# Performance work log

Hardware: AMD Instinct MI355X
Metric: run time of the kernel (lower is better)

Reference implementation:

```python
import jax, jax.numpy as jnp
import numpy as np
import math

N_HEAD = 16
D_MODEL = 1024
ATT_DIM = D_MODEL // N_HEAD


def setup_inputs() -> dict:
    key = jax.random.key(0)
    ks = jax.random.split(key, 11)
    B, T, D = 2, 2048, D_MODEL
    s = 1.0 / math.sqrt(D)
    return {
        "q": jax.random.normal(ks[0], (B, T, D), jnp.float32),
        "k": jax.random.normal(ks[1], (B, T, D), jnp.float32),
        "v": jax.random.normal(ks[2], (B, T, D), jnp.float32),
        "Wq": jax.random.normal(ks[3], (D, D), jnp.float32) * s,
        "bq": jnp.zeros((D,), jnp.float32),
        "Wk": jax.random.normal(ks[4], (D, D), jnp.float32) * s,
        "bk": jnp.zeros((D,), jnp.float32),
        "Wv": jax.random.normal(ks[5], (D, D), jnp.float32) * s,
        "bv": jnp.zeros((D,), jnp.float32),
        "Wo": jax.random.normal(ks[6], (D, D), jnp.float32) * s,
        "bo": jnp.zeros((D,), jnp.float32),
    }


def reference(q, k, v, Wq, bq, Wk, bk, Wv, bv, Wo, bo):
    B, T, D = q.shape
    H, hd = N_HEAD, ATT_DIM
    # Linear projections (torch Linear: x @ W.T + b)
    qh = (q @ Wq.T + bq).reshape(B, T, H, hd).transpose(0, 2, 1, 3)  # [B,H,T,hd]
    kh = (k @ Wk.T + bk).reshape(B, T, H, hd).transpose(0, 2, 1, 3)
    vh = (v @ Wv.T + bv).reshape(B, T, H, hd).transpose(0, 2, 1, 3)
    scale = 1.0 / math.sqrt(hd)
    score = jnp.einsum("bhqd,bhkd->bhqk", qh, kh) * scale  # [B,H,T,T]
    attn = jax.nn.softmax(score, axis=-1)
    out = jnp.einsum("bhqk,bhkd->bhqd", attn, vh)  # [B,H,T,hd]
    out = out.transpose(0, 2, 1, 3).reshape(B, T, D)
    return out @ Wo.T + bo
```

## Files before the change

kernel.cpp:

```cpp
#include <hip/hip_runtime.h>


typedef __attribute__((ext_vector_type(8))) short bf16x8;
typedef __attribute__((ext_vector_type(4))) float f32x4;
typedef __attribute__((ext_vector_type(4))) unsigned int u32x4;

#define E22 ((size_t)1 << 22)
#define E20 ((size_t)1 << 20)

__device__ __forceinline__ unsigned short f2bf(float x) {
    unsigned int u = __float_as_uint(x);
    u += 0x7fffu + ((u >> 16) & 1u);
    return (unsigned short)(u >> 16);
}
__device__ __forceinline__ unsigned int pk2bf(float a, float b) {
    return __builtin_amdgcn_perm(__float_as_uint(a), __float_as_uint(b), 0x03020706u);
}
__device__ __forceinline__ void gl16(const void* g, void* l) {
    __builtin_amdgcn_global_load_lds(
        (const __attribute__((address_space(1))) void*)g,
        (__attribute__((address_space(3))) void*)l, 16, 0, 0);
}
__device__ __forceinline__ f32x4 mfma16(bf16x8 a, bf16x8 b, f32x4 c) {
    return __builtin_amdgcn_mfma_f32_16x16x32_bf16(a, b, c, 0, 0, 0);
}

__global__ __launch_bounds__(256)
void split_all(const float* __restrict__ q, const float* __restrict__ k,
               const float* __restrict__ v, const float* __restrict__ wq,
               const float* __restrict__ wk, const float* __restrict__ wv,
               const float* __restrict__ wo, unsigned short* __restrict__ ws)
{
    const size_t t = (size_t)blockIdx.x * 256 + threadIdx.x;
    const size_t e = t * 4;
    const float* src; unsigned short* dst; size_t off;
    if (e < 3 * E22) {
        const unsigned int which = (unsigned int)(e >> 22);
        src = which == 0 ? q : (which == 1 ? k : v);
        off = e & (E22 - 1);
        dst = ws + (size_t)which * E22;
    } else {
        const size_t e2 = e - 3 * E22;
        const unsigned int which = (unsigned int)(e2 >> 20);
        off = e2 & (E20 - 1);
        src = which == 0 ? wq : (which == 1 ? wk : (which == 2 ? wv : wo));
        dst = ws + 3 * E22 + (size_t)which * E20;
    }
    const float4 xv = *(const float4*)(src + off);
    ushort4 h4;
    h4.x = f2bf(xv.x); h4.y = f2bf(xv.y); h4.z = f2bf(xv.z); h4.w = f2bf(xv.w);
    *(ushort4*)(dst + off) = h4;
}

__global__ __launch_bounds__(512)
void gemm_qkv(const unsigned short* __restrict__ Xall,
              const unsigned short* __restrict__ Wcat,
              const float* __restrict__ bq, const float* __restrict__ bk,
              const float* __restrict__ bv, unsigned short* __restrict__ Qhp,
              unsigned short* __restrict__ Khp, unsigned short* __restrict__ Vtp)
{
    __shared__ unsigned short Xs[3 * 4096], Ws[3 * 4096];
    const int tid = threadIdx.x;
    const int w = tid >> 6, ln = tid & 63;
    const int quad = ln >> 4, L = ln & 15;
    const int wy = w >> 1, wx = w & 1;

    const int bid = blockIdx.x;
    const int xcd = bid & 7, j = bid >> 3;
    const int gg = xcd * 12 + (j >> 3);
    const int which = gg >> 5, m_i = gg & 31, n_i = j & 7;
    const int m0 = m_i * 128;

    const unsigned short* X = Xall + (size_t)which * E22;
    const unsigned short* W = Wcat + ((size_t)which * 1024 + n_i * 128) * 1024;
    const float* bp = which == 0 ? bq : (which == 1 ? bk : bv);
    unsigned short* outp = which == 0 ? Qhp : (which == 1 ? Khp : Vtp);
    const float qscale = which == 0 ? 0.18033688011f : 1.0f;

    const int ci  = w * 64 + ln;
    const int row = ci >> 2;
    const int gc  = (ci & 3) ^ ((row >> 1) & 3);
    const int lb  = w * 1024;
    const unsigned short* Xbp = X + (size_t)m0 * 1024;
    const size_t gx = (size_t)row * 1024 + gc * 8;

    f32x4 acc[2][4];
#pragma unroll
    for (int i = 0; i < 2; ++i)
#pragma unroll
        for (int jj = 0; jj < 4; ++jj) { f32x4 z = {0.f,0.f,0.f,0.f}; acc[i][jj] = z; }

#define QSTAGE(k0_, bo_)                                                       \
    do {                                                                       \
        gl16(Xbp + gx + (k0_), (char*)Xs + (bo_) + lb);                        \
        gl16(W   + gx + (k0_), (char*)Ws + (bo_) + lb);                        \
    } while (0)

#define QCOMP(eo_)                                                             \
    do {                                                                       \
        const unsigned short* Xc = Xs + (eo_);                                 \
        const unsigned short* Wc = Ws + (eo_);                                 \
        bf16x8 ah[2], bh[4];                                                   \
        _Pragma("unroll")                                                      \
        for (int mt = 0; mt < 2; ++mt) {                                       \
            const int rr = wy * 32 + mt * 16 + L;                              \
            ah[mt] = *(const bf16x8*)(Xc + rr * 32 +                           \
                                      ((quad ^ ((rr >> 1) & 3)) * 8));         \
        }                                                                      \
        _Pragma("unroll")                                                      \
        for (int nt = 0; nt < 4; ++nt) {                                       \
            const int rr = wx * 64 + nt * 16 + L;                              \
            bh[nt] = *(const bf16x8*)(Wc + rr * 32 +                           \
                                      ((quad ^ ((rr >> 1) & 3)) * 8));         \
        }                                                                      \
        _Pragma("unroll")                                                      \
        for (int mt = 0; mt < 2; ++mt)                                         \
            _Pragma("unroll")                                                  \
            for (int nt = 0; nt < 4; ++nt)                                     \
                acc[mt][nt] = mfma16(ah[mt], bh[nt], acc[mt][nt]);             \
    } while (0)

    QSTAGE(0, 0);
    QSTAGE(32, 8192);

    int cur = 0;
    for (int kt = 0; kt < 31; ++kt) {
        asm volatile("s_waitcnt vmcnt(2)" ::: "memory");
        __builtin_amdgcn_s_barrier();
        asm volatile("" ::: "memory");
        if (kt < 30) {
            int st = cur + 2; if (st >= 3) st -= 3;
            QSTAGE((kt + 2) * 32, st * 8192);
        }
        QCOMP(cur * 4096);
        cur = (cur == 2) ? 0 : cur + 1;
    }
    asm volatile("s_waitcnt vmcnt(0)" ::: "memory");
    __builtin_amdgcn_s_barrier();
    asm volatile("" ::: "memory");
    QCOMP(cur * 4096);
#undef QSTAGE
#undef QCOMP

#pragma unroll
    for (int mt = 0; mt < 2; ++mt)
#pragma unroll
        for (int nt = 0; nt < 4; ++nt) {
            const int gm0 = m0 + wy * 32 + mt * 16 + quad * 4;
            const int bn  = n_i * 128 + wx * 64 + nt * 16 + L;
            const float bvv = bp[bn];
            const int hh = bn >> 6, dd = bn & 63;
            if (which < 2) {
#pragma unroll
                for (int r = 0; r < 4; ++r) {
                    const int gm = gm0 + r;
                    const int bb = gm >> 11, tt = gm & 2047;
                    outp[((size_t)(bb * 16 + hh) * 2048 + tt) * 64 + dd] =
                        f2bf((acc[mt][nt][r] + bvv) * qscale);
                }
            } else {
                const int bb = gm0 >> 11, t0 = gm0 & 2047;
                const int c5 = t0 & 31;
                const int p0 = (t0 & ~31) | (((c5 & 15) >> 2) << 3) | ((c5 >> 4) << 2);
                ushort4 pk;
                pk.x = f2bf(acc[mt][nt][0] + bvv);
                pk.y = f2bf(acc[mt][nt][1] + bvv);
                pk.z = f2bf(acc[mt][nt][2] + bvv);
                pk.w = f2bf(acc[mt][nt][3] + bvv);
                *(ushort4*)(outp + ((size_t)(bb * 16 + hh) * 64 + dd) * 2048 + p0) = pk;
            }
        }
}

__global__ __launch_bounds__(256)
void gemm_out(const unsigned short* __restrict__ X, const unsigned short* __restrict__ W,
              const float* __restrict__ bias, float* __restrict__ outp)
{
    __shared__ unsigned short Xs[3 * 4096], Ws[3 * 2048];
    const int tid = threadIdx.x;
    const int w = tid >> 6, ln = tid & 63;
    const int quad = ln >> 4, L = ln & 15;

    const int bid = blockIdx.x;
    const int xcd = bid & 7, j = bid >> 3;
    const int m0 = (xcd * 4 + (j >> 4)) * 128;
    const int n0 = (j & 15) * 64;

    const int cix0 = ln, cix1 = 64 + ln;
    const int rowx0 = w * 32 + (cix0 >> 2), rowx1 = w * 32 + (cix1 >> 2);
    const int gcx0 = (cix0 & 3) ^ ((rowx0 >> 1) & 3);
    const int gcx1 = (cix1 & 3) ^ ((rowx1 >> 1) & 3);
    const int roww = w * 16 + (ln >> 2);
    const int gcw = (ln & 3) ^ ((roww >> 1) & 3);
    const size_t gxx0 = (size_t)(m0 + rowx0) * 1024 + gcx0 * 8;
    const size_t gxx1 = (size_t)(m0 + rowx1) * 1024 + gcx1 * 8;
    const size_t gww  = (size_t)(n0 + roww) * 1024 + gcw * 8;

    f32x4 acc[2][4];
#pragma unroll
    for (int i = 0; i < 2; ++i)
#pragma unroll
        for (int jj = 0; jj < 4; ++jj) { f32x4 z = {0.f,0.f,0.f,0.f}; acc[i][jj] = z; }

#define OSTAGE(k0_, bf_)                                                       \
    do {                                                                       \
        gl16(X + gxx0 + (k0_), (char*)Xs + (bf_) * 8192 + w * 2048);           \
        gl16(X + gxx1 + (k0_), (char*)Xs + (bf_) * 8192 + w * 2048 + 1024);    \
        gl16(W + gww  + (k0_), (char*)Ws + (bf_) * 4096 + w * 1024);           \
    } while (0)

#define OCOMP(bf_)                                                             \
    do {                                                                       \
        const unsigned short* Xc = Xs + (bf_) * 4096;                          \
        const unsigned short* Wc = Ws + (bf_) * 2048;                          \
        bf16x8 ah[2], bh[4];                                                   \
        _Pragma("unroll")                                                      \
        for (int mt = 0; mt < 2; ++mt) {                                       \
            const int row = w * 32 + mt * 16 + L;                              \
            ah[mt] = *(const bf16x8*)(Xc + row * 32 +                          \
                                      ((quad ^ ((row >> 1) & 3)) * 8));        \
        }                                                                      \
        _Pragma("unroll")                                                      \
        for (int nt = 0; nt < 4; ++nt) {                                       \
            const int row = nt * 16 + L;                                       \
            bh[nt] = *(const bf16x8*)(Wc + row * 32 +                          \
                                      ((quad ^ ((row >> 1) & 3)) * 8));        \
        }                                                                      \
        _Pragma("unroll")                                                      \
        for (int mt = 0; mt < 2; ++mt)                                         \
            _Pragma("unroll")                                                  \
            for (int nt = 0; nt < 4; ++nt)                                     \
                acc[mt][nt] = mfma16(ah[mt], bh[nt], acc[mt][nt]);             \
    } while (0)

    OSTAGE(0, 0);
    OSTAGE(32, 1);

    int cur = 0;
    for (int kt = 0; kt < 31; ++kt) {
        asm volatile("s_waitcnt vmcnt(3)" ::: "memory");
        __builtin_amdgcn_s_barrier();
        asm volatile("" ::: "memory");
        if (kt < 30) {
            int st = cur + 2; if (st >= 3) st -= 3;
            OSTAGE((kt + 2) * 32, st);
        }
        OCOMP(cur);
        cur = (cur == 2) ? 0 : cur + 1;
    }
    asm volatile("s_waitcnt vmcnt(0)" ::: "memory");
    __builtin_amdgcn_s_barrier();
    asm volatile("" ::: "memory");
    OCOMP(cur);
#undef OSTAGE
#undef OCOMP

#pragma unroll
    for (int mt = 0; mt < 2; ++mt)
#pragma unroll
        for (int nt = 0; nt < 4; ++nt) {
            const int gm0 = m0 + w * 32 + mt * 16 + quad * 4;
            const int gn  = n0 + nt * 16 + L;
            const float bvv = bias[gn];
#pragma unroll
            for (int r = 0; r < 4; ++r)
                outp[(size_t)(gm0 + r) * 1024 + gn] = acc[mt][nt][r] + bvv;
        }
}

__global__ __launch_bounds__(256, 2)
void flash(const unsigned short* __restrict__ Qh, const unsigned short* __restrict__ Kh,
           const unsigned short* __restrict__ Vt, unsigned short* __restrict__ A)
{
    __shared__ unsigned short SM[32768];
    __shared__ float Lsc[2 * 4 * 64];
    const int tid = threadIdx.x;
    const int w = tid >> 6, ln = tid & 63;
    const int quad = ln >> 4, L = ln & 15;
    const int wq = w & 1, wk = w >> 1;

    const int bid = blockIdx.x;
    const int xcd = bid & 7, j = bid >> 3;
    const int bh_i = xcd * 4 + (j & 3);
    const int qt = j >> 2;
    const int b = bh_i >> 4, h = bh_i & 15;

    const unsigned short* Qb = Qh + ((size_t)bh_i * 2048 + qt * 128 + wq * 64) * 64;
    const unsigned short* Kb = Kh + (size_t)bh_i * 2048 * 64;
    const unsigned short* Vb = Vt + (size_t)bh_i * 64 * 2048;

    bf16x8 bq[4][2];
#pragma unroll
    for (int nt = 0; nt < 4; ++nt)
#pragma unroll
        for (int kc = 0; kc < 2; ++kc)
            bq[nt][kc] = *(const bf16x8*)(Qb + (nt * 16 + L) * 64 + kc * 32 + quad * 8);

    const short one_bf = (short)0x3F80;
    bf16x8 bone = {one_bf, one_bf, one_bf, one_bf, one_bf, one_bf, one_bf, one_bf};

    f32x4 o[4][4];
    f32x4 lacc[4];
#pragma unroll
    for (int mtd = 0; mtd < 4; ++mtd)
#pragma unroll
        for (int nt = 0; nt < 4; ++nt) { f32x4 z = {0.f,0.f,0.f,0.f}; o[mtd][nt] = z; }
#pragma unroll
    for (int nt = 0; nt < 4; ++nt) { f32x4 z = {0.f,0.f,0.f,0.f}; lacc[nt] = z; }

    const int ci0 = (w * 2 + 0) * 64 + ln, ci1 = (w * 2 + 1) * 64 + ln;
    const int rr0 = ci0 >> 3, rr1 = ci1 >> 3;
    const int gc0 = (ci0 & 7) ^ (rr0 & 7), gc1 = (ci1 & 7) ^ (rr1 & 7);

#define STAGE1(kt_, b_, s_)                                                     \
    do {                                                                        \
        gl16(Kb + (size_t)((kt_) * 64 + rr0) * 64 + gc0 * 8,                    \
             (char*)SM + (b_) * 16384 + (s_) * 8192 + (w * 2 + 0) * 1024);      \
        gl16(Kb + (size_t)((kt_) * 64 + rr1) * 64 + gc1 * 8,                    \
             (char*)SM + (b_) * 16384 + (s_) * 8192 + (w * 2 + 1) * 1024);      \
        gl16(Vb + (size_t)rr0 * 2048 + (kt_) * 64 + gc0 * 8,                    \
             (char*)SM + 32768 + (b_) * 16384 + (s_) * 8192 + (w * 2 + 0) * 1024); \
        gl16(Vb + (size_t)rr1 * 2048 + (kt_) * 64 + gc1 * 8,                    \
             (char*)SM + 32768 + (b_) * 16384 + (s_) * 8192 + (w * 2 + 1) * 1024); \
    } while (0)

#define SUBCOMP(b_, s_)                                                         \
    do {                                                                        \
        const unsigned short* Ksb = SM + (b_) * 8192 + (s_) * 4096;             \
        const unsigned short* Vsb = SM + 16384 + (b_) * 8192 + (s_) * 4096;     \
        bf16x8 ak[2][2];                                                        \
        _Pragma("unroll")                                                       \
        for (int mt = 0; mt < 2; ++mt)                                          \
            _Pragma("unroll")                                                   \
            for (int kc = 0; kc < 2; ++kc) {                                    \
                const int row = wk * 32 + mt * 16 + L;                          \
                ak[mt][kc] = *(const bf16x8*)(Ksb + row * 64 +                  \
                                              (((kc * 4 + quad) ^ (L & 7)) * 8)); \
            }                                                                   \
        f32x4 s[2][4];                                                          \
        _Pragma("unroll")                                                       \
        for (int mt = 0; mt < 2; ++mt)                                          \
            _Pragma("unroll")                                                   \
            for (int nt = 0; nt < 4; ++nt) {                                    \
                f32x4 z = {0.f, 0.f, 0.f, 0.f};                                 \
                z = mfma16(ak[mt][0], bq[nt][0], z);                            \
                z = mfma16(ak[mt][1], bq[nt][1], z);                            \
                s[mt][nt] = z;                                                  \
            }                                                                   \
        bf16x8 pbx[4];                                                          \
        _Pragma("unroll")                                                       \
        for (int nt = 0; nt < 4; ++nt) {                                        \
            u32x4 pd;                                                           \
            pd.x = pk2bf(__builtin_amdgcn_exp2f(s[0][nt][0]),                   \
                         __builtin_amdgcn_exp2f(s[0][nt][1]));                  \
            pd.y = pk2bf(__builtin_amdgcn_exp2f(s[0][nt][2]),                   \
                         __builtin_amdgcn_exp2f(s[0][nt][3]));                  \
            pd.z = pk2bf(__builtin_amdgcn_exp2f(s[1][nt][0]),                   \
                         __builtin_amdgcn_exp2f(s[1][nt][1]));                  \
            pd.w = pk2bf(__builtin_amdgcn_exp2f(s[1][nt][2]),                   \
                         __builtin_amdgcn_exp2f(s[1][nt][3]));                  \
            pbx[nt] = __builtin_bit_cast(bf16x8, pd);                           \
        }                                                                       \
        bf16x8 av[4];                                                           \
        _Pragma("unroll")                                                       \
        for (int mtd = 0; mtd < 4; ++mtd) {                                     \
            const int row = mtd * 16 + L;                                       \
            av[mtd] = *(const bf16x8*)(Vsb + row * 64 +                         \
                                       (((wk * 4 + quad) ^ (L & 7)) * 8));      \
        }                                                                       \
        _Pragma("unroll")                                                       \
        for (int mtd = 0; mtd < 4; ++mtd)                                       \
            _Pragma("unroll")                                                   \
            for (int nt = 0; nt < 4; ++nt)                                      \
                o[mtd][nt] = mfma16(av[mtd], pbx[nt], o[mtd][nt]);              \
        _Pragma("unroll")                                                       \
        for (int nt = 0; nt < 4; ++nt)                                          \
            lacc[nt] = mfma16(bone, pbx[nt], lacc[nt]);                         \
    } while (0)

    STAGE1(0, 0, 0);
    STAGE1(1, 0, 1);

    for (int p = 0; p < 16; ++p) {
        const int cur = p & 1;
        __syncthreads();
        if (p < 15) {
            STAGE1(2 * p + 2, cur ^ 1, 0);
            STAGE1(2 * p + 3, cur ^ 1, 1);
        }
        SUBCOMP(cur, 0);
        SUBCOMP(cur, 1);
    }
#undef STAGE1
#undef SUBCOMP

    __syncthreads();
    float* Rb = (float*)SM;
    if (wk == 1) {
#pragma unroll
        for (int mtd = 0; mtd < 4; ++mtd)
#pragma unroll
            for (int nt = 0; nt < 4; ++nt)
                *(f32x4*)(Rb + wq * 4096 + (mtd * 4 + nt) * 256 + ln * 4) = o[mtd][nt];
#pragma unroll
        for (int nt = 0; nt < 4; ++nt)
            Lsc[wq * 256 + nt * 64 + ln] = lacc[nt][0];
    }
    __syncthreads();
    if (wk == 0) {
#pragma unroll
        for (int mtd = 0; mtd < 4; ++mtd)
#pragma unroll
            for (int nt = 0; nt < 4; ++nt)
                o[mtd][nt] += *(const f32x4*)(Rb + wq * 4096 + (mtd * 4 + nt) * 256 + ln * 4);

#pragma unroll
        for (int nt = 0; nt < 4; ++nt) {
            const float lsum = lacc[nt][0] + Lsc[wq * 256 + nt * 64 + ln];
            const float inv = 1.0f / lsum;
            const int qrow = b * 2048 + qt * 128 + wq * 64 + nt * 16 + L;
#pragma unroll
            for (int mtd = 0; mtd < 4; ++mtd) {
                const int d0 = mtd * 16 + quad * 4;
                ushort4 pk;
                pk.x = f2bf(o[mtd][nt][0] * inv);
                pk.y = f2bf(o[mtd][nt][1] * inv);
                pk.z = f2bf(o[mtd][nt][2] * inv);
                pk.w = f2bf(o[mtd][nt][3] * inv);
                *(ushort4*)(A + (size_t)qrow * 1024 + h * 64 + d0) = pk;
            }
        }
    }
}

extern "C" void kernel_launch(void* const* d_in, const int* in_sizes, int n_in,
                              void* d_out, int out_size, void* d_ws, size_t ws_size,
                              hipStream_t stream) {
    const float* q  = (const float*)d_in[0];
    const float* k  = (const float*)d_in[1];
    const float* v  = (const float*)d_in[2];
    const float* Wq = (const float*)d_in[3];
    const float* bq = (const float*)d_in[4];
    const float* Wk = (const float*)d_in[5];
    const float* bk = (const float*)d_in[6];
    const float* Wv = (const float*)d_in[7];
    const float* bv = (const float*)d_in[8];
    const float* Wo = (const float*)d_in[9];
    const float* bo = (const float*)d_in[10];

    unsigned short* W = (unsigned short*)d_ws;
    unsigned short *Xall = W;
    unsigned short *Wcat = W + 3 * E22;
    unsigned short *Wob  = Wcat + 3 * E20;
    unsigned short *Qhp  = W + 4 * E22;
    unsigned short *Khp  = W + 5 * E22;
    unsigned short *Vtp  = W + 6 * E22;
    unsigned short *A    = W;

    split_all<<<16384, 256, 0, stream>>>(q, k, v, Wq, Wk, Wv, Wo, W);

    gemm_qkv<<<768, 512, 0, stream>>>(Xall, Wcat, bq, bk, bv, Qhp, Khp, Vtp);

    flash<<<512, 256, 0, stream>>>(Qhp, Khp, Vtp, A);

    gemm_out<<<512, 256, 0, stream>>>(A, Wob, bo, (float*)d_out);
}
```

Baseline: 218.0 us.

## Shrink QKV GEMM tile to 128x64 with 256 threads and double buffering

The QKV projection GEMM moves from 512-thread blocks with 128x128 tiles and a three-stage async pipeline to 256-thread blocks with 128x64 tiles and two-stage double buffering, doubling the grid to 1536 blocks. The XCD-aware block mapping and load indexing are reworked to match. The intent is more blocks per CU and better load balance, at the cost of less reuse of each X tile, more global traffic, and a shallower pipeline that waits on every load with a full __syncthreads.

```diff
diff --git a/kernel.cpp b/kernel.cpp
--- a/kernel.cpp
+++ b/kernel.cpp
@@ -52,37 +52,42 @@
     *(ushort4*)(dst + off) = h4;
 }
 
-__global__ __launch_bounds__(512)
+__global__ __launch_bounds__(256)
 void gemm_qkv(const unsigned short* __restrict__ Xall,
               const unsigned short* __restrict__ Wcat,
               const float* __restrict__ bq, const float* __restrict__ bk,
               const float* __restrict__ bv, unsigned short* __restrict__ Qhp,
               unsigned short* __restrict__ Khp, unsigned short* __restrict__ Vtp)
 {
-    __shared__ unsigned short Xs[3 * 4096], Ws[3 * 4096];
+    __shared__ unsigned short Xs[2 * 4096], Ws[2 * 2048];
     const int tid = threadIdx.x;
     const int w = tid >> 6, ln = tid & 63;
     const int quad = ln >> 4, L = ln & 15;
-    const int wy = w >> 1, wx = w & 1;
 
     const int bid = blockIdx.x;
-    const int xcd = bid & 7, j = bid >> 3;
-    const int gg = xcd * 12 + (j >> 3);
-    const int which = gg >> 5, m_i = gg & 31, n_i = j & 7;
+    const int xcd = bid & 7;
+    const int g = xcd * 192 + (bid >> 3);
+    const int which = g >> 9;
+    const int rem = g & 511;
+    const int m_i = rem >> 4, n_i = rem & 15;
     const int m0 = m_i * 128;
 
     const unsigned short* X = Xall + (size_t)which * E22;
-    const unsigned short* W = Wcat + ((size_t)which * 1024 + n_i * 128) * 1024;
+    const unsigned short* W = Wcat + ((size_t)which * 1024 + n_i * 64) * 1024;
     const float* bp = which == 0 ? bq : (which == 1 ? bk : bv);
     unsigned short* outp = which == 0 ? Qhp : (which == 1 ? Khp : Vtp);
     const float qscale = which == 0 ? 0.18033688011f : 1.0f;
 
-    const int ci  = w * 64 + ln;
-    const int row = ci >> 2;
-    const int gc  = (ci & 3) ^ ((row >> 1) & 3);
-    const int lb  = w * 1024;
+    const int cix0 = ln, cix1 = 64 + ln;
+    const int rowx0 = w * 32 + (cix0 >> 2), rowx1 = w * 32 + (cix1 >> 2);
+    const int gcx0 = (cix0 & 3) ^ ((rowx0 >> 1) & 3);
+    const int gcx1 = (cix1 & 3) ^ ((rowx1 >> 1) & 3);
+    const int roww = w * 16 + (ln >> 2);
+    const int gcw = (ln & 3) ^ ((roww >> 1) & 3);
     const unsigned short* Xbp = X + (size_t)m0 * 1024;
-    const size_t gx = (size_t)row * 1024 + gc * 8;
+    const size_t gxx0 = (size_t)rowx0 * 1024 + gcx0 * 8;
+    const size_t gxx1 = (size_t)rowx1 * 1024 + gcx1 * 8;
+    const size_t gww  = (size_t)roww * 1024 + gcw * 8;
 
     f32x4 acc[2][4];
 #pragma unroll
@@ -90,28 +95,29 @@
 #pragma unroll
         for (int jj = 0; jj < 4; ++jj) { f32x4 z = {0.f,0.f,0.f,0.f}; acc[i][jj] = z; }
 
-#define QSTAGE(k0_, bo_)                                                       \
+#define QSTAGE(kt_, bf_)                                                       \
     do {                                                                       \
-        gl16(Xbp + gx + (k0_), (char*)Xs + (bo_) + lb);                        \
-        gl16(W   + gx + (k0_), (char*)Ws + (bo_) + lb);                        \
-    } while (0)
-
-#define QCOMP(eo_)                                                             \
+        gl16(Xbp + gxx0 + (kt_) * 32, (char*)Xs + (bf_) * 8192 + w * 2048);    \
+        gl16(Xbp + gxx1 + (kt_) * 32, (char*)Xs + (bf_) * 8192 + w * 2048 + 1024); \
+        gl16(W + gww + (kt_) * 32,    (char*)Ws + (bf_) * 4096 + w * 1024);    \
+    } while (0)
+
+#define QCOMP(bf_)                                                             \
     do {                                                                       \
-        const unsigned short* Xc = Xs + (eo_);                                 \
-        const unsigned short* Wc = Ws + (eo_);                                 \
+        const unsigned short* Xc = Xs + (bf_) * 4096;                          \
+        const unsigned short* Wc = Ws + (bf_) * 2048;                          \
         bf16x8 ah[2], bh[4];                                                   \
         _Pragma("unroll")                                                      \
         for (int mt = 0; mt < 2; ++mt) {                                       \
-            const int rr = wy * 32 + mt * 16 + L;                              \
-            ah[mt] = *(const bf16x8*)(Xc + rr * 32 +                           \
-                                      ((quad ^ ((rr >> 1) & 3)) * 8));         \
+            const int row = w * 32 + mt * 16 + L;                              \
+            ah[mt] = *(const bf16x8*)(Xc + row * 32 +                          \
+                                      ((quad ^ ((row >> 1) & 3)) * 8));        \
         }                                                                      \
         _Pragma("unroll")                                                      \
         for (int nt = 0; nt < 4; ++nt) {                                       \
-            const int rr = wx * 64 + nt * 16 + L;                              \
-            bh[nt] = *(const bf16x8*)(Wc + rr * 32 +                           \
-                                      ((quad ^ ((rr >> 1) & 3)) * 8));         \
+            const int row = nt * 16 + L;                                       \
+            bh[nt] = *(const bf16x8*)(Wc + row * 32 +                          \
+                                      ((quad ^ ((row >> 1) & 3)) * 8));        \
         }                                                                      \
         _Pragma("unroll")                                                      \
         for (int mt = 0; mt < 2; ++mt)                                         \
@@ -121,24 +127,13 @@
     } while (0)
 
     QSTAGE(0, 0);
-    QSTAGE(32, 8192);
-
-    int cur = 0;
-    for (int kt = 0; kt < 31; ++kt) {
-        asm volatile("s_waitcnt vmcnt(2)" ::: "memory");
-        __builtin_amdgcn_s_barrier();
-        asm volatile("" ::: "memory");
-        if (kt < 30) {
-            int st = cur + 2; if (st >= 3) st -= 3;
-            QSTAGE((kt + 2) * 32, st * 8192);
-        }
-        QCOMP(cur * 4096);
-        cur = (cur == 2) ? 0 : cur + 1;
-    }
-    asm volatile("s_waitcnt vmcnt(0)" ::: "memory");
-    __builtin_amdgcn_s_barrier();
-    asm volatile("" ::: "memory");
-    QCOMP(cur * 4096);
+
+    for (int kt = 0; kt < 32; ++kt) {
+        const int cur = kt & 1;
+        __syncthreads();
+        if (kt < 31) QSTAGE(kt + 1, cur ^ 1);
+        QCOMP(cur);
+    }
 #undef QSTAGE
 #undef QCOMP
 
@@ -146,8 +141,8 @@
     for (int mt = 0; mt < 2; ++mt)
 #pragma unroll
         for (int nt = 0; nt < 4; ++nt) {
-            const int gm0 = m0 + wy * 32 + mt * 16 + quad * 4;
-            const int bn  = n_i * 128 + wx * 64 + nt * 16 + L;
+            const int gm0 = m0 + w * 32 + mt * 16 + quad * 4;
+            const int bn  = n_i * 64 + nt * 16 + L;
             const float bvv = bp[bn];
             const int hh = bn >> 6, dd = bn & 63;
             if (which < 2) {
@@ -459,7 +454,7 @@
 
     split_all<<<16384, 256, 0, stream>>>(q, k, v, Wq, Wk, Wv, Wo, W);
 
-    gemm_qkv<<<768, 512, 0, stream>>>(Xall, Wcat, bq, bk, bv, Qhp, Khp, Vtp);
+    gemm_qkv<<<1536, 256, 0, stream>>>(Xall, Wcat, bq, bk, bv, Qhp, Khp, Vtp);
 
     flash<<<512, 256, 0, stream>>>(Qhp, Khp, Vtp, A);
 
```

Result: slower. 223.2 us (+2.4%).
